# Kernel optimization log

Measured on AMD Instinct MI355X. Metric: run time of the kernel, lower is better.

## Reference

```python
import jax, jax.numpy as jnp
import numpy as np
import math

V = 32768; H = 768; NH = 12; D = 64; L = 12; I = 2048
S = 512; B = 8; BK = 32; MAXP = 512; EPS = 1e-7
STD = math.sqrt(2.0 / (5.0 * H))
SCALE = 1.0 / math.sqrt(3 * D)


def _bucket_positions(seq_len):
    # static numpy: DeBERTa-style log-bucketed relative positions
    rel = np.arange(seq_len)[:, None] - np.arange(seq_len)[None, :]
    sign = np.sign(rel)
    mid = BK // 2
    abs_pos = np.where((rel < mid) & (rel > -mid), mid - 1, np.minimum(np.abs(rel), MAXP - 1))
    log_pos = np.ceil(np.log(abs_pos / mid) / math.log((MAXP - 1) / mid) * (mid - 1)).astype(np.int64) + mid
    bucket = np.where(abs_pos <= mid, rel, log_pos * sign).astype(np.int64)
    return bucket + BK - 1  # [S, S] in [0, 2*BK-2]


def _ln(x):
    # LayerNorm without affine params (elementwise_affine=False)
    m = jnp.mean(x, axis=-1, keepdims=True)
    v = jnp.var(x, axis=-1, keepdims=True)
    return (x - m) * jax.lax.rsqrt(v + EPS)


def _forward(input_ids, attention_mask, word_emb, rel_emb, rel_g, rel_b,
             Wqk, bqk, Wvg, bvg, Wout, bout, W1, W2):
    pos_idx = jnp.asarray(_bucket_positions(S))      # [S, S]
    x = _ln(word_emb[input_ids])                     # [S, B, H]
    rel = _ln(rel_emb) * rel_g + rel_b               # [2*BK-1, H] (affine LN)
    mask = attention_mask                            # [B, 1, 1, S] bool, True = masked
    for i in range(L):
        # ---- disentangled attention ----
        hs = _ln(x)
        qk = jnp.einsum('sbh,oh->sbo', hs, Wqk[i]) + bqk[i]
        q, k = jnp.split(qk, 2, axis=-1)
        vg = jnp.einsum('sbh,oh->sbo', hs, Wvg[i]) + bvg[i]
        v, g = jnp.split(vg, 2, axis=-1)
        g = jax.nn.gelu(g, approximate=False)
        pos = jnp.einsum('rh,oh->ro', rel, Wqk[i]) + bqk[i]   # [2*BK-1, 2H]
        posg = pos[pos_idx]                                   # [S, S, 2H]
        qpos, kpos = jnp.split(posg, 2, axis=-1)
        qpos = qpos.reshape(S, S, NH, D)
        kpos = kpos.reshape(S, S, NH, D)
        qh = q.reshape(S, B, NH, D)
        kh = k.reshape(S, B, NH, D)
        vh = v.reshape(S, B, NH, D)
        scores = jnp.einsum('qbhd,kbhd->bhqk', qh, kh) * SCALE          # content-content
        scores = scores + jnp.einsum('qbhd,qkhd->bhqk', qh, kpos) * SCALE  # content-position
        scores = scores + jnp.einsum('kbhd,qkhd->bhqk', kh, qpos) * SCALE  # position-content
        s = jnp.where(mask, -1e9, scores)
        p = jax.nn.softmax(s, axis=-1)
        p = jnp.where(mask, 0.0, p)
        ctx = jnp.einsum('bhqk,kbhd->qbhd', p, vh).reshape(S, B, H)
        ctx = _ln(ctx * g)
        ctx = jnp.einsum('sbh,oh->sbo', ctx, Wout[i]) + bout[i]
        x = x + ctx
        # ---- GeGLU feed-forward ----
        h = _ln(x)
        h = jnp.einsum('sbh,oh->sbo', h, W1[i])   # [S, B, 2I]
        a, gt = jnp.split(h, 2, axis=-1)
        h = _ln(a * jax.nn.gelu(gt, approximate=True))
        h = jnp.einsum('sbi,oi->sbo', h, W2[i])
        x = x + h
    return x


def setup_inputs() -> dict:
    key = jax.random.key(0)
    ks = jax.random.split(key, 12)
    def nrm(k, shape):
        return (jax.random.normal(k, shape) * STD).astype(jnp.float32)
    return {
        'input_ids': jax.random.randint(ks[0], (S, B), 0, V),
        'attention_mask': jax.random.randint(ks[1], (B, 1, 1, S), 0, 2).astype(bool),
        'word_emb': nrm(ks[2], (V, H)),
        'rel_emb': nrm(ks[3], (2 * BK - 1, H)),
        'rel_g': jnp.ones((H,), jnp.float32),
        'rel_b': jnp.zeros((H,), jnp.float32),
        'Wqk': nrm(ks[4], (L, 2 * H, H)),
        'bqk': jnp.zeros((L, 2 * H), jnp.float32),
        'Wvg': nrm(ks[5], (L, 2 * H, H)),
        'bvg': jnp.zeros((L, 2 * H), jnp.float32),
        'Wout': nrm(ks[6], (L, H, H)),
        'bout': jnp.zeros((L, H), jnp.float32),
        'W1': nrm(ks[7], (L, 2 * I, H)),
        'W2': nrm(ks[8], (L, H, I)),
    }


def reference(input_ids, attention_mask, word_emb, rel_emb, rel_g, rel_b,
              Wqk, bqk, Wvg, bvg, Wout, bout, W1, W2):
    return _forward(input_ids, attention_mask, word_emb, rel_emb, rel_g, rel_b,
                    Wqk, bqk, Wvg, bvg, Wout, bout, W1, W2)
```

## Files before the change

kernel.cpp:

```cpp
#include <hip/hip_runtime.h>
#include <math.h>

#define SS 512
#define BB 8
#define NHH 12
#define DD 64
#define HH 768
#define II 2048
#define LL 12
#define SCALE_F 0.07216878364870323f

typedef __attribute__((ext_vector_type(8))) short bf16x8;
typedef __attribute__((ext_vector_type(4))) float f32x4;

__device__ __forceinline__ unsigned short f2b(float f) {
    union { float f; unsigned int u; } x; x.f = f;
    unsigned int r = x.u + 0x7fffu + ((x.u >> 16) & 1u);
    return (unsigned short)(r >> 16);
}
__device__ __forceinline__ float b2f(unsigned short u) {
    union { unsigned int u; float f; } x; x.u = ((unsigned int)u) << 16;
    return x.f;
}

__device__ __forceinline__ float2 blockReduceSum2(float a, float b) {
    __shared__ float2 sm[4];
    __shared__ float2 bc;
#pragma unroll
    for (int o = 32; o > 0; o >>= 1) {
        a += __shfl_down(a, o);
        b += __shfl_down(b, o);
    }
    int t = threadIdx.x;
    if ((t & 63) == 0) sm[t >> 6] = make_float2(a, b);
    __syncthreads();
    if (t == 0) {
        float xa = sm[0].x + sm[1].x + sm[2].x + sm[3].x;
        float xb = sm[0].y + sm[1].y + sm[2].y + sm[3].y;
        bc = make_float2(xa, xb);
    }
    __syncthreads();
    return bc;
}

__device__ __forceinline__ float gelu_erf(float v) {
    return 0.5f * v * (1.0f + erff(v * 0.70710678118654752f));
}
__device__ __forceinline__ float gelu_tanh(float v) {
    const float c = 0.7978845608028654f;
    return 0.5f * v * (1.0f + tanhf(c * (v + 0.044715f * v * v * v)));
}

__global__ __launch_bounds__(256) void k_decode_mask(const unsigned char* __restrict__ raw,
                                                     int* __restrict__ mask, int n) {
    __shared__ int s_any;
    if (threadIdx.x == 0) s_any = 0;
    __syncthreads();
    int local = 0;
    for (int i = threadIdx.x; i < n; i += blockDim.x)
        if ((i & 3) && raw[i]) local = 1;
    if (local) atomicOr(&s_any, 1);
    __syncthreads();
    bool isU8 = (s_any != 0);
    const int* as_int = (const int*)raw;
    for (int i = threadIdx.x; i < n; i += blockDim.x)
        mask[i] = isU8 ? (raw[i] != 0) : (as_int[i] != 0);
}

__global__ __launch_bounds__(256) void k_bucket(int* __restrict__ tab) {
    int i = blockIdx.x * 256 + threadIdx.x;
    if (i >= 1023) return;
    int rel = i - 511;
    int a = rel < 0 ? -rel : rel;
    int abs_pos = (a < 16) ? 15 : (a < 511 ? a : 511);
    int bucket;
    if (abs_pos <= 16) {
        bucket = rel;
    } else {
        double lp = ceil(log((double)abs_pos / 16.0) / log(511.0 / 16.0) * 15.0);
        int l = (int)lp + 16;
        bucket = (rel > 0) ? l : -l;
    }
    int idx = bucket + 31;
    if (idx < 0) idx = 0;
    if (idx > 62) idx = 62;
    tab[i] = idx;
}

__global__ __launch_bounds__(256) void k_f2b(const float* __restrict__ in,
                                             unsigned short* __restrict__ out, int n8) {
    int i = blockIdx.x * 256 + threadIdx.x;
    if (i >= n8) return;
    float4 a = ((const float4*)in)[2 * (size_t)i];
    float4 b = ((const float4*)in)[2 * (size_t)i + 1];
    ushort4 lo, hi;
    lo.x = f2b(a.x); lo.y = f2b(a.y); lo.z = f2b(a.z); lo.w = f2b(a.w);
    hi.x = f2b(b.x); hi.y = f2b(b.y); hi.z = f2b(b.z); hi.w = f2b(b.w);
    ((ushort4*)out)[2 * (size_t)i] = lo;
    ((ushort4*)out)[2 * (size_t)i + 1] = hi;
}

__global__ __launch_bounds__(256) void k_f2b_ln(const float* __restrict__ wvg,
                                                const float* __restrict__ wout,
                                                const float* __restrict__ w1,
                                                const float* __restrict__ w2,
                                                unsigned short* __restrict__ wbf,
                                                const float* __restrict__ x,
                                                unsigned short* __restrict__ hs) {
    int bid = blockIdx.x;
    int t = threadIdx.x;
    if (bid < 3169) {
        int i = bid * 256 + t;
        if (i >= 811008) return;
        const float* src;
        int off;
        if (i < 221184) {
            if (i < 147456) { src = wvg;  off = i; }
            else            { src = wout; off = i - 147456; }
        } else if (i < 614400) { src = w1; off = i - 221184; }
        else                   { src = w2; off = i - 614400; }
        float4 a = ((const float4*)src)[2 * (size_t)off];
        float4 b = ((const float4*)src)[2 * (size_t)off + 1];
        ushort4 lo, hi;
        lo.x = f2b(a.x); lo.y = f2b(a.y); lo.z = f2b(a.z); lo.w = f2b(a.w);
        hi.x = f2b(b.x); hi.y = f2b(b.y); hi.z = f2b(b.z); hi.w = f2b(b.w);
        ((ushort4*)wbf)[2 * (size_t)i] = lo;
        ((ushort4*)wbf)[2 * (size_t)i + 1] = hi;
    } else {
        int row = bid - 3169;
        const float* r = x + (size_t)row * HH;
        float v0 = r[t], v1 = r[t + 256], v2 = r[t + 512];
        float s = v0 + v1 + v2;
        float ss = v0 * v0 + v1 * v1 + v2 * v2;
        float2 r2 = blockReduceSum2(s, ss);
        float mean = r2.x * (1.0f / HH);
        float var = r2.y * (1.0f / HH) - mean * mean;
        float rs = rsqrtf(var + 1e-7f);
        unsigned short* o = hs + (size_t)row * HH;
        o[t] = f2b((v0 - mean) * rs);
        o[t + 256] = f2b((v1 - mean) * rs);
        o[t + 512] = f2b((v2 - mean) * rs);
    }
}

__global__ __launch_bounds__(256) void k_ln_bf(const float* __restrict__ in,
                                               unsigned short* __restrict__ out) {
    int row = blockIdx.x, t = threadIdx.x;
    const float* r = in + (size_t)row * HH;
    float v0 = r[t], v1 = r[t + 256], v2 = r[t + 512];
    float s = v0 + v1 + v2;
    float ss = v0 * v0 + v1 * v1 + v2 * v2;
    float2 r2 = blockReduceSum2(s, ss);
    float mean = r2.x * (1.0f / HH);
    float var = r2.y * (1.0f / HH) - mean * mean;
    float rs = rsqrtf(var + 1e-7f);
    unsigned short* o = out + (size_t)row * HH;
    o[t] = f2b((v0 - mean) * rs);
    o[t + 256] = f2b((v1 - mean) * rs);
    o[t + 512] = f2b((v2 - mean) * rs);
}

__global__ __launch_bounds__(256) void k_embed_ln(const int* __restrict__ ids,
                                                  const float* __restrict__ emb,
                                                  float* __restrict__ out) {
    int row = blockIdx.x, t = threadIdx.x;
    const float* r = emb + (size_t)ids[row] * HH;
    float v0 = r[t], v1 = r[t + 256], v2 = r[t + 512];
    float s = v0 + v1 + v2;
    float ss = v0 * v0 + v1 * v1 + v2 * v2;
    float2 r2 = blockReduceSum2(s, ss);
    float mean = r2.x * (1.0f / HH);
    float var = r2.y * (1.0f / HH) - mean * mean;
    float rs = rsqrtf(var + 1e-7f);
    float* o = out + (size_t)row * HH;
    o[t] = (v0 - mean) * rs;
    o[t + 256] = (v1 - mean) * rs;
    o[t + 512] = (v2 - mean) * rs;
}

__global__ __launch_bounds__(256) void k_rel_ln_bf(const float* __restrict__ rel_emb,
                                                   const float* __restrict__ g,
                                                   const float* __restrict__ b,
                                                   unsigned short* __restrict__ out) {
    int row = blockIdx.x, t = threadIdx.x;
    unsigned short* o = out + (size_t)row * HH;
    if (row >= 63) {
        o[t] = 0; o[t + 256] = 0; o[t + 512] = 0;
        return;
    }
    const float* r = rel_emb + (size_t)row * HH;
    float v0 = r[t], v1 = r[t + 256], v2 = r[t + 512];
    float s = v0 + v1 + v2;
    float ss = v0 * v0 + v1 * v1 + v2 * v2;
    float2 r2 = blockReduceSum2(s, ss);
    float mean = r2.x * (1.0f / HH);
    float var = r2.y * (1.0f / HH) - mean * mean;
    float rs = rsqrtf(var + 1e-7f);
    o[t] = f2b((v0 - mean) * rs * g[t] + b[t]);
    o[t + 256] = f2b((v1 - mean) * rs * g[t + 256] + b[t + 256]);
    o[t + 512] = f2b((v2 - mean) * rs * g[t + 512] + b[t + 512]);
}

__global__ __launch_bounds__(256) void k_gated_ln(const float* __restrict__ ctxr,
                                                  const unsigned short* __restrict__ qkvg,
                                                  unsigned short* __restrict__ out) {
    int row = blockIdx.x, t = threadIdx.x;
    const float* cr = ctxr + (size_t)row * HH;
    const unsigned short* gr = qkvg + (size_t)row * 3072 + 2304;
    float v[3];
    float s = 0.f, ss = 0.f;
#pragma unroll
    for (int e = 0; e < 3; ++e) {
        int i = t + e * 256;
        float x = cr[i] * gelu_erf(b2f(gr[i]));
        v[e] = x;
        s += x; ss += x * x;
    }
    float2 r2 = blockReduceSum2(s, ss);
    float mean = r2.x * (1.0f / HH);
    float var = r2.y * (1.0f / HH) - mean * mean;
    float rs = rsqrtf(var + 1e-7f);
    unsigned short* o = out + (size_t)row * HH;
#pragma unroll
    for (int e = 0; e < 3; ++e) o[t + e * 256] = f2b((v[e] - mean) * rs);
}

__global__ __launch_bounds__(256) void k_ffn_ln(const unsigned short* __restrict__ ffh,
                                                unsigned short* __restrict__ out) {
    int row = blockIdx.x, t = threadIdx.x;
    const unsigned short* ar = ffh + (size_t)row * 4096 + t * 8;
    const unsigned short* gr = ar + II;
    ushort4 a0 = *(const ushort4*)ar;
    ushort4 a1 = *(const ushort4*)(ar + 4);
    ushort4 g0 = *(const ushort4*)gr;
    ushort4 g1 = *(const ushort4*)(gr + 4);
    float av[8] = {b2f(a0.x), b2f(a0.y), b2f(a0.z), b2f(a0.w),
                   b2f(a1.x), b2f(a1.y), b2f(a1.z), b2f(a1.w)};
    float gv[8] = {b2f(g0.x), b2f(g0.y), b2f(g0.z), b2f(g0.w),
                   b2f(g1.x), b2f(g1.y), b2f(g1.z), b2f(g1.w)};
    float v[8];
    float s = 0.f, ss = 0.f;
#pragma unroll
    for (int e = 0; e < 8; ++e) {
        float x = av[e] * gelu_tanh(gv[e]);
        v[e] = x;
        s += x; ss += x * x;
    }
    float2 r2 = blockReduceSum2(s, ss);
    float mean = r2.x * (1.0f / II);
    float var = r2.y * (1.0f / II) - mean * mean;
    float rs = rsqrtf(var + 1e-7f);
    ushort4 o0, o1;
    o0.x = f2b((v[0] - mean) * rs); o0.y = f2b((v[1] - mean) * rs);
    o0.z = f2b((v[2] - mean) * rs); o0.w = f2b((v[3] - mean) * rs);
    o1.x = f2b((v[4] - mean) * rs); o1.y = f2b((v[5] - mean) * rs);
    o1.z = f2b((v[6] - mean) * rs); o1.w = f2b((v[7] - mean) * rs);
    unsigned short* o = out + (size_t)row * II + t * 8;
    *(ushort4*)o = o0;
    *(ushort4*)(o + 4) = o1;
}

template <int OBF>
__global__ __launch_bounds__(256) void k_gemm_bf16(const unsigned short* __restrict__ A, int lda,
                                                   const unsigned short* __restrict__ W, int ldw,
                                                   void* __restrict__ Cv, int ldc,
                                                   int M, int N, int K,
                                                   const float* __restrict__ bias,
                                                   const float* __restrict__ bias2,
                                                   const float* __restrict__ res,
                                                   size_t wz, size_t cz, size_t bz) {
    __shared__ unsigned short As[128 * 32];
    __shared__ unsigned short Ws[128 * 32];
    int zz = blockIdx.z;
    W += (size_t)zz * wz;
    if (bias) bias += (size_t)zz * bz;
    int nwg = gridDim.x * gridDim.y;
    int orig = blockIdx.y * gridDim.x + blockIdx.x;
    int qq = nwg >> 3, rr = nwg & 7;
    int xcd = orig & 7, idx = orig >> 3;
    int wg = (xcd < rr ? xcd * (qq + 1) : rr * (qq + 1) + (xcd - rr) * qq) + idx;
    int bx = wg % gridDim.x, by = wg / gridDim.x;

    const int t = threadIdx.x;
    const int lane = t & 63, wid = t >> 6;
    const int row0 = by * 128, col0 = bx * 128;
    const int wr = (wid >> 1) * 64, wc = (wid & 1) * 64;
    const int rA = lane & 15, kA = (lane >> 4) * 8;

    f32x4 acc[4][4] = {};

    for (int k0 = 0; k0 < K; k0 += 32) {
#pragma unroll
        for (int j = 0; j < 2; ++j) {
            int c = t + j * 256;
            int r = c >> 2, ko = (c & 3) * 8;
            const unsigned short* srcA = A + (size_t)(row0 + r) * lda + k0 + ko;
            const unsigned short* srcB = W + (size_t)(col0 + r) * ldw + k0 + ko;
            unsigned short* dstA = As + (size_t)(j * 256 + wid * 64) * 8;
            unsigned short* dstB = Ws + (size_t)(j * 256 + wid * 64) * 8;
            __builtin_amdgcn_global_load_lds(
                (const __attribute__((address_space(1))) void*)srcA,
                (__attribute__((address_space(3))) void*)dstA, 16, 0, 0);
            __builtin_amdgcn_global_load_lds(
                (const __attribute__((address_space(1))) void*)srcB,
                (__attribute__((address_space(3))) void*)dstB, 16, 0, 0);
        }
        __syncthreads();
        bf16x8 af[4], bfr[4];
#pragma unroll
        for (int m = 0; m < 4; ++m)
            af[m] = *(const bf16x8*)&As[(wr + m * 16 + rA) * 32 + kA];
#pragma unroll
        for (int n = 0; n < 4; ++n)
            bfr[n] = *(const bf16x8*)&Ws[(wc + n * 16 + rA) * 32 + kA];
#pragma unroll
        for (int m = 0; m < 4; ++m)
#pragma unroll
            for (int n = 0; n < 4; ++n)
                acc[m][n] = __builtin_amdgcn_mfma_f32_16x16x32_bf16(af[m], bfr[n], acc[m][n], 0, 0, 0);
        __syncthreads();
    }

    float* Cf = (float*)Cv + (size_t)zz * cz;
    unsigned short* Cb = (unsigned short*)Cv + (size_t)zz * cz;
    const int cl = lane & 15, rg = (lane >> 4) * 4;
#pragma unroll
    for (int n = 0; n < 4; ++n) {
        int gc = col0 + wc + n * 16 + cl;
        float bv = 0.0f;
        if (bias) bv = (bias2 && gc >= 1536) ? bias2[gc - 1536] : bias[gc];
#pragma unroll
        for (int m = 0; m < 4; ++m) {
#pragma unroll
            for (int i = 0; i < 4; ++i) {
                int gr = row0 + wr + m * 16 + rg + i;
                float v = acc[m][n][i] + bv;
                if (OBF) {
                    Cb[(size_t)gr * ldc + gc] = f2b(v);
                } else {
                    if (res) v += res[(size_t)gr * ldc + gc];
                    Cf[(size_t)gr * ldc + gc] = v;
                }
            }
        }
    }
}

#define SKSLOT 16384

__device__ __forceinline__ void sk_stage(const unsigned short* __restrict__ Ab, int lda,
                                         const unsigned short* __restrict__ Wb, int ldw,
                                         unsigned char* slot, int t, int wid) {
    int rit = t >> 3;
    int kb = (t & 7) << 4;
#pragma unroll
    for (int c = 0; c < 2; ++c) {
        int row = c * 32 + rit;
        int gkb = kb ^ ((row & 7) << 4);
        const unsigned short* src = Ab + (size_t)row * lda + (gkb >> 1);
        unsigned char* dst = slot + c * 4096 + wid * 1024;
        __builtin_amdgcn_global_load_lds(
            (const __attribute__((address_space(1))) void*)src,
            (__attribute__((address_space(3))) void*)dst, 16, 0, 0);
    }
#pragma unroll
    for (int c = 0; c < 2; ++c) {
        int row = c * 32 + rit;
        int gkb = kb ^ ((row & 7) << 4);
        const unsigned short* src = Wb + (size_t)row * ldw + (gkb >> 1);
        unsigned char* dst = slot + 8192 + c * 4096 + wid * 1024;
        __builtin_amdgcn_global_load_lds(
            (const __attribute__((address_space(1))) void*)src,
            (__attribute__((address_space(3))) void*)dst, 16, 0, 0);
    }
}

__device__ __forceinline__ void sk_compute(const unsigned char* slot, int wr, int wc,
                                           int rA, int g16, f32x4 acc[2][2]) {
    const unsigned char* Ab = slot;
    const unsigned char* Bb = slot + 8192;
    bf16x8 a[2][2], b[2][2];
#pragma unroll
    for (int m = 0; m < 2; ++m) {
        int row = wr + m * 16 + rA;
        int sw = (row & 7) << 4;
#pragma unroll
        for (int s = 0; s < 2; ++s)
            a[m][s] = *(const bf16x8*)(Ab + row * 128 + ((s * 64 + g16 * 16) ^ sw));
    }
#pragma unroll
    for (int n = 0; n < 2; ++n) {
        int row = wc + n * 16 + rA;
        int sw = (row & 7) << 4;
#pragma unroll
        for (int s = 0; s < 2; ++s)
            b[n][s] = *(const bf16x8*)(Bb + row * 128 + ((s * 64 + g16 * 16) ^ sw));
    }
    __builtin_amdgcn_s_setprio(1);
#pragma unroll
    for (int m = 0; m < 2; ++m)
#pragma unroll
        for (int n = 0; n < 2; ++n) {
            acc[m][n] = __builtin_amdgcn_mfma_f32_16x16x32_bf16(a[m][0], b[n][0], acc[m][n], 0, 0, 0);
            acc[m][n] = __builtin_amdgcn_mfma_f32_16x16x32_bf16(a[m][1], b[n][1], acc[m][n], 0, 0, 0);
        }
    __builtin_amdgcn_s_setprio(0);
}

__global__ __launch_bounds__(256) void k_gemm_skinny(const unsigned short* __restrict__ A, int lda,
                                                     const unsigned short* __restrict__ W, int ldw,
                                                     float* __restrict__ C, int ldc,
                                                     int M, int N, int K,
                                                     const float* __restrict__ bias,
                                                     const float* __restrict__ res) {
    __shared__ unsigned char smem[2 * SKSLOT];
    int nwg = gridDim.x * gridDim.y;
    int orig = blockIdx.y * gridDim.x + blockIdx.x;
    int qq = nwg >> 3, rr = nwg & 7;
    int xcd = orig & 7, idx = orig >> 3;
    int wg = (xcd < rr ? xcd * (qq + 1) : rr * (qq + 1) + (xcd - rr) * qq) + idx;
    int bx = wg % gridDim.x, by = wg / gridDim.x;

    const int t = threadIdx.x;
    const int lane = t & 63, wid = t >> 6;
    const int row0 = by * 64, col0 = bx * 64;
    const int wr = (wid >> 1) * 32, wc = (wid & 1) * 32;
    const int rA = lane & 15, g16 = lane >> 4;
    const unsigned short* Abase = A + (size_t)row0 * lda;
    const unsigned short* Wbase = W + (size_t)col0 * ldw;

    const int nt = K >> 6;
    f32x4 acc[2][2] = {};

    sk_stage(Abase, lda, Wbase, ldw, smem, t, wid);

    for (int tt = 0; tt < nt; ++tt) {
        asm volatile("s_barrier" ::: "memory");
        if (tt + 1 < nt) {
            sk_stage(Abase + (size_t)(tt + 1) * 64, lda, Wbase + (size_t)(tt + 1) * 64,
                     ldw, smem + (size_t)((tt + 1) & 1) * SKSLOT, t, wid);
            asm volatile("s_waitcnt vmcnt(4)" ::: "memory");
        } else {
            asm volatile("s_waitcnt vmcnt(0)" ::: "memory");
        }
        asm volatile("s_barrier" ::: "memory");
        sk_compute(smem + (size_t)(tt & 1) * SKSLOT, wr, wc, rA, g16, acc);
    }

    const int cl = lane & 15, rg = (lane >> 4) * 4;
#pragma unroll
    for (int n = 0; n < 2; ++n) {
        int gc = col0 + wc + n * 16 + cl;
        float bv = bias ? bias[gc] : 0.0f;
#pragma unroll
        for (int m = 0; m < 2; ++m) {
#pragma unroll
            for (int i = 0; i < 4; ++i) {
                int gr = row0 + wr + m * 16 + rg + i;
                float v = acc[m][n][i] + bv;
                if (res) v += res[(size_t)gr * ldc + gc];
                C[(size_t)gr * ldc + gc] = v;
            }
        }
    }
}

#define GSLOT 49152

__device__ __forceinline__ void g_stage(const unsigned short* __restrict__ Abase, int lda,
                                        const unsigned short* __restrict__ Wbase, int ldw,
                                        unsigned char* slot, int t, int wid) {
    int rit = t >> 3;
    int kb = (t & 7) << 4;
#pragma unroll
    for (int c = 0; c < 2; ++c) {
        int row = c * 64 + rit;
        int gkb = kb ^ ((row & 7) << 4);
        const unsigned short* src = Abase + (size_t)row * lda + (gkb >> 1);
        unsigned char* dst = slot + c * 8192 + wid * 1024;
        __builtin_amdgcn_global_load_lds(
            (const __attribute__((address_space(1))) void*)src,
            (__attribute__((address_space(3))) void*)dst, 16, 0, 0);
    }
#pragma unroll
    for (int c = 0; c < 4; ++c) {
        int row = c * 64 + rit;
        int gkb = kb ^ ((row & 7) << 4);
        const unsigned short* src = Wbase + (size_t)row * ldw + (gkb >> 1);
        unsigned char* dst = slot + 16384 + c * 8192 + wid * 1024;
        __builtin_amdgcn_global_load_lds(
            (const __attribute__((address_space(1))) void*)src,
            (__attribute__((address_space(3))) void*)dst, 16, 0, 0);
    }
}

__device__ __forceinline__ void g_compute(const unsigned char* slot, int wm, int wn,
                                          int rA, int g16, f32x4 acc[4][4]) {
    const unsigned char* Ab = slot;
    const unsigned char* Bb = slot + 16384;
    bf16x8 a[4][2], b[4][2];
#pragma unroll
    for (int m = 0; m < 4; ++m) {
        int row = wm * 64 + m * 16 + rA;
        int sw = (row & 7) << 4;
#pragma unroll
        for (int s = 0; s < 2; ++s)
            a[m][s] = *(const bf16x8*)(Ab + row * 128 + ((s * 64 + g16 * 16) ^ sw));
    }
#pragma unroll
    for (int n = 0; n < 4; ++n) {
        int row = wn * 64 + n * 16 + rA;
        int sw = (row & 7) << 4;
#pragma unroll
        for (int s = 0; s < 2; ++s)
            b[n][s] = *(const bf16x8*)(Bb + row * 128 + ((s * 64 + g16 * 16) ^ sw));
    }
    __builtin_amdgcn_s_setprio(1);
#pragma unroll
    for (int m = 0; m < 4; ++m)
#pragma unroll
        for (int n = 0; n < 4; ++n) {
            acc[m][n] = __builtin_amdgcn_mfma_f32_16x16x32_bf16(a[m][0], b[n][0], acc[m][n], 0, 0, 0);
            acc[m][n] = __builtin_amdgcn_mfma_f32_16x16x32_bf16(a[m][1], b[n][1], acc[m][n], 0, 0, 0);
        }
    __builtin_amdgcn_s_setprio(0);
}

template <int OBF>
__global__ __launch_bounds__(512, 1) void k_gemm_big(const unsigned short* __restrict__ A, int lda,
                                                     const unsigned short* __restrict__ W,
                                                     const unsigned short* __restrict__ Wb2, int ldw,
                                                     void* __restrict__ Cv, int ldc,
                                                     int M, int N, int K,
                                                     const float* __restrict__ bias,
                                                     const float* __restrict__ bias2,
                                                     const float* __restrict__ res) {
    extern __shared__ unsigned char smem[];
    int nwg = gridDim.x * gridDim.y;
    int orig = blockIdx.y * gridDim.x + blockIdx.x;
    int qq = nwg >> 3, rr = nwg & 7;
    int xcd = orig & 7, idx = orig >> 3;
    int wg = (xcd < rr ? xcd * (qq + 1) : rr * (qq + 1) + (xcd - rr) * qq) + idx;
    int bx = wg % gridDim.x, by = wg / gridDim.x;

    const int t = threadIdx.x;
    const int lane = t & 63, wid = t >> 6;
    const int wm = wid >> 2, wn = wid & 3;
    const int rA = lane & 15, g16 = lane >> 4;
    const int row0 = by * 128, col0 = bx * 256;
    const unsigned short* Abase = A + (size_t)row0 * lda;
    const unsigned short* Wbase = (Wb2 && col0 >= 1536)
                                      ? Wb2 + (size_t)(col0 - 1536) * ldw
                                      : W + (size_t)col0 * ldw;

    const int nt = K >> 6;
    f32x4 acc[4][4] = {};

    g_stage(Abase, lda, Wbase, ldw, smem, t, wid);
    g_stage(Abase + 64, lda, Wbase + 64, ldw, smem + GSLOT, t, wid);

#define GBAR() asm volatile("s_barrier" ::: "memory")
#define GITER(T, STG, VMSTR)                                                        \
    do {                                                                            \
        GBAR();                                                                     \
        if (STG)                                                                    \
            g_stage(Abase + (size_t)(T + 2) * 64, lda, Wbase + (size_t)(T + 2) * 64,\
                    ldw, smem + (size_t)((T + 2) % 3) * GSLOT, t, wid);             \
        asm volatile(VMSTR ::: "memory");                                           \
        GBAR();                                                                     \
        g_compute(smem + (size_t)((T) % 3) * GSLOT, wm, wn, rA, g16, acc);          \
    } while (0)

    int tt = 0;
    for (; tt < nt - 2; ++tt) GITER(tt, true, "s_waitcnt vmcnt(12)");
    GITER(tt, false, "s_waitcnt vmcnt(6)");
    ++tt;
    GITER(tt, false, "s_waitcnt vmcnt(0)");
#undef GITER
#undef GBAR

    float* Cf = (float*)Cv;
    unsigned short* Cb = (unsigned short*)Cv;
    const int cl = lane & 15, rg = (lane >> 4) * 4;
#pragma unroll
    for (int n = 0; n < 4; ++n) {
        int gc = col0 + wn * 64 + n * 16 + cl;
        float bv = 0.0f;
        if (bias) bv = (bias2 && gc >= 1536) ? bias2[gc - 1536] : bias[gc];
#pragma unroll
        for (int m = 0; m < 4; ++m) {
#pragma unroll
            for (int i = 0; i < 4; ++i) {
                int gr = row0 + wm * 64 + m * 16 + rg + i;
                float v = acc[m][n][i] + bv;
                if (OBF) {
                    Cb[(size_t)gr * ldc + gc] = f2b(v);
                } else {
                    if (res) v += res[(size_t)gr * ldc + gc];
                    Cf[(size_t)gr * ldc + gc] = v;
                }
            }
        }
    }
}

__global__ __launch_bounds__(256) void k_repack_cppc(const unsigned short* __restrict__ qkvg,
                                                     const unsigned short* __restrict__ pp,
                                                     unsigned short* __restrict__ qT,
                                                     unsigned short* __restrict__ kT,
                                                     unsigned short* __restrict__ vT,
                                                     float* __restrict__ cp,
                                                     float* __restrict__ pc) {
    __shared__ unsigned char shmem[12288];
    int t = threadIdx.x;
    if (blockIdx.x < 8) {
        unsigned short (*tile)[72] = (unsigned short(*)[72])shmem;
        int bh = blockIdx.y;
        int b = bh / NHH, h = bh % NHH;
        int s0 = blockIdx.x * 64;
#pragma unroll
        for (int j = 0; j < 2; ++j) {
            int idx = t + j * 256;
            int r = idx >> 3, dc = idx & 7;
            const unsigned short* src = qkvg + ((size_t)(s0 + r) * BB + b) * 3072 + h * DD + dc * 8;
            ushort4 a = *(const ushort4*)src;
            ushort4 c = *(const ushort4*)(src + 4);
            unsigned short* dq = qT + ((size_t)bh * SS + s0 + r) * DD + dc * 8;
            *(ushort4*)dq = a; *(ushort4*)(dq + 4) = c;
            const unsigned short* srck = src + HH;
            ushort4 a2 = *(const ushort4*)srck;
            ushort4 c2 = *(const ushort4*)(srck + 4);
            unsigned short* dk = kT + ((size_t)bh * SS + s0 + r) * DD + dc * 8;
            *(ushort4*)dk = a2; *(ushort4*)(dk + 4) = c2;
        }
#pragma unroll
        for (int j = 0; j < 4; ++j) {
            int idx = t + j * 256;
            int r = idx >> 4, c4 = idx & 15;
            ushort4 u = *(const ushort4*)(qkvg + ((size_t)(s0 + r) * BB + b) * 3072 + 1536 + h * DD + c4 * 4);
            *(ushort4*)&tile[r][c4 * 4] = u;
        }
        __syncthreads();
#pragma unroll
        for (int j = 0; j < 2; ++j) {
            int idx = t + j * 256;
            int d = idx >> 3, s8 = idx & 7;
            ushort4 a, c;
            a.x = tile[s8 * 8 + 0][d]; a.y = tile[s8 * 8 + 1][d];
            a.z = tile[s8 * 8 + 2][d]; a.w = tile[s8 * 8 + 3][d];
            c.x = tile[s8 * 8 + 4][d]; c.y = tile[s8 * 8 + 5][d];
            c.z = tile[s8 * 8 + 6][d]; c.w = tile[s8 * 8 + 7][d];
            unsigned short* dst = vT + ((size_t)bh * DD + d) * SS + s0 + s8 * 8;
            *(ushort4*)dst = a; *(ushort4*)(dst + 4) = c;
        }
    } else {
        int cid = (blockIdx.x - 8) * 96 + blockIdx.y;
        int z = cid >= 384;
        int rem = cid - (z ? 384 : 0);
        int h = rem >> 5;
        int mt = rem & 31;
        int aoff = z ? HH : 0;
        int toff = z ? 0 : HH;
        float* out = z ? pc : cp;
        unsigned short* As = (unsigned short*)shmem;
        unsigned short* Bs = (unsigned short*)(shmem + 8192);
        const int lane = t & 63, wid = t >> 6;
        const int rA = lane & 15, kA = (lane >> 4) * 8;

        f32x4 acc[2][4] = {};

        for (int k0 = 0; k0 < 64; k0 += 32) {
#pragma unroll
            for (int j = 0; j < 2; ++j) {
                int c = t + j * 256;
                int r = c >> 2, ko = (c & 3) * 8;
                const unsigned short* srcA = qkvg + (size_t)(mt * 128 + r) * 3072 + aoff + h * DD + k0 + ko;
                unsigned short* dstA = As + (size_t)(j * 256 + wid * 64) * 8;
                __builtin_amdgcn_global_load_lds(
                    (const __attribute__((address_space(1))) void*)srcA,
                    (__attribute__((address_space(3))) void*)dstA, 16, 0, 0);
            }
            {
                int r = t >> 2, ko = (t & 3) * 8;
                const unsigned short* srcB = pp + (size_t)r * 1536 + toff + h * DD + k0 + ko;
                unsigned short* dstB = Bs + (size_t)(wid * 64) * 8;
                __builtin_amdgcn_global_load_lds(
                    (const __attribute__((address_space(1))) void*)srcB,
                    (__attribute__((address_space(3))) void*)dstB, 16, 0, 0);
            }
            __syncthreads();
            bf16x8 af[2], bfr[4];
#pragma unroll
            for (int m = 0; m < 2; ++m)
                af[m] = *(const bf16x8*)&As[(wid * 32 + m * 16 + rA) * 32 + kA];
#pragma unroll
            for (int n = 0; n < 4; ++n)
                bfr[n] = *(const bf16x8*)&Bs[(n * 16 + rA) * 32 + kA];
#pragma unroll
            for (int m = 0; m < 2; ++m)
#pragma unroll
                for (int n = 0; n < 4; ++n)
                    acc[m][n] = __builtin_amdgcn_mfma_f32_16x16x32_bf16(af[m], bfr[n], acc[m][n], 0, 0, 0);
            __syncthreads();
        }

        const int cl = lane & 15, rg = (lane >> 4) * 4;
#pragma unroll
        for (int m = 0; m < 2; ++m)
#pragma unroll
            for (int n = 0; n < 4; ++n) {
                int gc = n * 16 + cl;
                if (gc < 63) {
#pragma unroll
                    for (int i = 0; i < 4; ++i) {
                        int gr = mt * 128 + wid * 32 + m * 16 + rg + i;
                        int sIdx = gr >> 3, bIdx = gr & 7;
                        out[(((size_t)(bIdx * NHH + h)) * SS + sIdx) * 63 + gc] = acc[m][n][i];
                    }
                }
            }
    }
}

__global__ __launch_bounds__(256) void k_attn_fused(
    const unsigned short* __restrict__ qT, const unsigned short* __restrict__ kT,
    const unsigned short* __restrict__ vT, const float* __restrict__ cp,
    const float* __restrict__ pc, const int* __restrict__ bucket,
    const int* __restrict__ mask, float* __restrict__ ctxr) {
    __shared__ float cps[64 * 63];
    __shared__ float pcs[64 * 63];
    __shared__ unsigned short pb_all[4][16 * 72];
    __shared__ int btab[1023];
    int t = threadIdx.x;
    int lane = t & 63, wid = t >> 6;
    int bh = blockIdx.y;
    int b = bh / NHH, h = bh % NHH;
    int qb0 = blockIdx.x * 64;
    int q0 = qb0 + wid * 16;
    int rA = lane & 15, g = lane >> 4, kA = g * 8;
    unsigned short* pb = pb_all[wid];
    const unsigned short* qTb = qT + (size_t)bh * SS * DD;
    const unsigned short* kTb = kT + (size_t)bh * SS * DD;
    const unsigned short* vTb = vT + (size_t)bh * DD * SS;
    const float* cpb = cp + (size_t)bh * SS * 63 + (size_t)qb0 * 63;
    const float* pcb = pc + (size_t)bh * SS * 63;
    const int* mkb = mask + b * SS;

    for (int i = t; i < 1023; i += 256) btab[i] = bucket[i];
    for (int i = t; i < 1008; i += 256) ((float4*)cps)[i] = ((const float4*)cpb)[i];

    bf16x8 aq[2];
#pragma unroll
    for (int dc = 0; dc < 2; ++dc)
        aq[dc] = *(const bf16x8*)&qTb[(size_t)(q0 + rA) * DD + dc * 32 + kA];

    f32x4 o[4] = {};
    float mrow[4], lrow[4];
#pragma unroll
    for (int i = 0; i < 4; ++i) { mrow[i] = -INFINITY; lrow[i] = 0.f; }

    for (int kt = 0; kt < 8; ++kt) {
        int k0 = kt * 64;
        __syncthreads();
        {
            const float4* src = (const float4*)(pcb + (size_t)k0 * 63);
            for (int i = t; i < 1008; i += 256) ((float4*)pcs)[i] = src[i];
        }
        f32x4 sa[4] = {};
#pragma unroll
        for (int n = 0; n < 4; ++n) {
            bf16x8 bk0 = *(const bf16x8*)&kTb[(size_t)(k0 + n * 16 + rA) * DD + kA];
            bf16x8 bk1 = *(const bf16x8*)&kTb[(size_t)(k0 + n * 16 + rA) * DD + 32 + kA];
            sa[n] = __builtin_amdgcn_mfma_f32_16x16x32_bf16(aq[0], bk0, sa[n], 0, 0, 0);
            sa[n] = __builtin_amdgcn_mfma_f32_16x16x32_bf16(aq[1], bk1, sa[n], 0, 0, 0);
        }
        int mk[4];
#pragma unroll
        for (int n = 0; n < 4; ++n) mk[n] = mkb[k0 + n * 16 + rA];
        __syncthreads();

        float pv[4][4];
#pragma unroll
        for (int i = 0; i < 4; ++i) {
            int qr = wid * 16 + g * 4 + i;
            int q = qb0 + qr;
            float sv[4];
            float tmax = -INFINITY;
#pragma unroll
            for (int n = 0; n < 4; ++n) {
                int kr = n * 16 + rA;
                int id = btab[q - (k0 + kr) + 511];
                float v = (sa[n][i] + cps[qr * 63 + id] + pcs[kr * 63 + id]) * SCALE_F;
                v = mk[n] ? -1e9f : v;
                sv[n] = v;
                tmax = fmaxf(tmax, v);
            }
            tmax = fmaxf(tmax, __shfl_xor(tmax, 1, 16));
            tmax = fmaxf(tmax, __shfl_xor(tmax, 2, 16));
            tmax = fmaxf(tmax, __shfl_xor(tmax, 4, 16));
            tmax = fmaxf(tmax, __shfl_xor(tmax, 8, 16));
            float mold = mrow[i];
            float mnew = fmaxf(mold, tmax);
            float ls = 0.f;
#pragma unroll
            for (int n = 0; n < 4; ++n) {
                float p = __expf(sv[n] - mnew);
                pv[n][i] = p;
                ls += p;
            }
            ls += __shfl_xor(ls, 1, 16);
            ls += __shfl_xor(ls, 2, 16);
            ls += __shfl_xor(ls, 4, 16);
            ls += __shfl_xor(ls, 8, 16);
            if (mnew > mold) {
                float alpha = __expf(mold - mnew);
                lrow[i] = lrow[i] * alpha + ls;
                mrow[i] = mnew;
#pragma unroll
                for (int n = 0; n < 4; ++n) o[n][i] *= alpha;
            } else {
                lrow[i] += ls;
            }
        }
#pragma unroll
        for (int n = 0; n < 4; ++n)
#pragma unroll
            for (int i = 0; i < 4; ++i)
                pb[(g * 4 + i) * 72 + n * 16 + rA] = f2b(pv[n][i]);
        bf16x8 ap[2];
#pragma unroll
        for (int kc = 0; kc < 2; ++kc)
            ap[kc] = *(const bf16x8*)&pb[rA * 72 + kc * 32 + kA];
#pragma unroll
        for (int n = 0; n < 4; ++n) {
            bf16x8 bv0 = *(const bf16x8*)&vTb[(size_t)(n * 16 + rA) * SS + k0 + kA];
            bf16x8 bv1 = *(const bf16x8*)&vTb[(size_t)(n * 16 + rA) * SS + k0 + 32 + kA];
            o[n] = __builtin_amdgcn_mfma_f32_16x16x32_bf16(ap[0], bv0, o[n], 0, 0, 0);
            o[n] = __builtin_amdgcn_mfma_f32_16x16x32_bf16(ap[1], bv1, o[n], 0, 0, 0);
        }
    }
#pragma unroll
    for (int i = 0; i < 4; ++i) {
        int q = q0 + g * 4 + i;
        float inv = 1.0f / lrow[i];
#pragma unroll
        for (int n = 0; n < 4; ++n)
            ctxr[((size_t)q * BB + b) * HH + h * DD + n * 16 + rA] = o[n][i] * inv;
    }
}

static inline void gemm_big(const unsigned short* A, int lda,
                            const unsigned short* W, const unsigned short* Wb2, int ldw,
                            void* C, int ldc, int M, int N, int K,
                            const float* bias, const float* bias2, const float* res,
                            int obf, hipStream_t st) {
    dim3 g(N / 256, M / 128);
    if (obf)
        k_gemm_big<1><<<g, 512, 3 * GSLOT, st>>>(A, lda, W, Wb2, ldw, C, ldc, M, N, K, bias, bias2, res);
    else
        k_gemm_big<0><<<g, 512, 3 * GSLOT, st>>>(A, lda, W, Wb2, ldw, C, ldc, M, N, K, bias, bias2, res);
}

extern "C" void kernel_launch(void* const* d_in, const int* in_sizes, int n_in,
                              void* d_out, int out_size, void* d_ws, size_t ws_size,
                              hipStream_t stream) {
    static int attr_done = 0;
    if (!attr_done) {
        hipFuncSetAttribute((const void*)&k_gemm_big<1>,
                            hipFuncAttributeMaxDynamicSharedMemorySize, 3 * GSLOT);
        hipFuncSetAttribute((const void*)&k_gemm_big<0>,
                            hipFuncAttributeMaxDynamicSharedMemorySize, 3 * GSLOT);
        attr_done = 1;
    }

    const int* ids = (const int*)d_in[0];
    const unsigned char* maskraw = (const unsigned char*)d_in[1];
    const float* word_emb = (const float*)d_in[2];
    const float* rel_emb = (const float*)d_in[3];
    const float* rel_g = (const float*)d_in[4];
    const float* rel_b = (const float*)d_in[5];
    const float* Wqk = (const float*)d_in[6];
    const float* bqk = (const float*)d_in[7];
    const float* Wvg = (const float*)d_in[8];
    const float* bvg = (const float*)d_in[9];
    const float* Wout = (const float*)d_in[10];
    const float* bout = (const float*)d_in[11];
    const float* W1 = (const float*)d_in[12];
    const float* W2 = (const float*)d_in[13];

    const size_t N_X = (size_t)SS * BB * HH;
    const size_t N_CP = (size_t)SS * BB * NHH * 63;
    const size_t N_H2 = (size_t)SS * BB * II;
    const size_t N_WQK = (size_t)2 * HH * HH;
    const size_t N_WOUT = (size_t)HH * HH;
    const size_t N_W1 = (size_t)2 * II * HH;
    const size_t N_W2 = (size_t)HH * II;
    const size_t N_HD = (size_t)BB * NHH * SS * DD;
    const size_t N_QKVG = (size_t)SS * BB * 3072;
    const size_t N_FFH = (size_t)SS * BB * 4096;
    const size_t N_PP = (size_t)128 * 1536;

    float* ws = (float*)d_ws;
    float* x = ws;
    float* ctxr = x + N_X;
    float* cp = ctxr + N_X;
    float* pc = cp + N_CP;
    unsigned short* us = (unsigned short*)(pc + N_CP);
    unsigned short* qkvg = us;
    unsigned short* hs_bf = qkvg + N_QKVG;
    unsigned short* ctx_bf = hs_bf + N_X;
    unsigned short* h2_bf = ctx_bf + N_X;
    unsigned short* ffh = h2_bf + N_H2;
    unsigned short* wqk_all = ffh + N_FFH;
    unsigned short* wvg_bf = wqk_all + 12 * N_WQK;
    unsigned short* wout_bf = wvg_bf + N_WQK;
    unsigned short* w1_bf = wout_bf + N_WOUT;
    unsigned short* w2_bf = w1_bf + N_W1;
    unsigned short* ppall = w2_bf + N_W2;
    unsigned short* rel_bf = ppall + 12 * N_PP;
    unsigned short* qT = rel_bf + 128 * HH;
    unsigned short* kT = qT + N_HD;
    unsigned short* vT = kT + N_HD;
    int* bucket = (int*)(vT + N_HD);
    int* maski = bucket + 1024;

    size_t need_bytes = ((size_t)(maski + BB * SS) - (size_t)d_ws);
    if (ws_size < need_bytes) return;

    k_decode_mask<<<1, 256, 0, stream>>>(maskraw, maski, BB * SS);
    k_bucket<<<4, 256, 0, stream>>>(bucket);
    k_embed_ln<<<SS * BB, 256, 0, stream>>>(ids, word_emb, x);
    k_rel_ln_bf<<<128, 256, 0, stream>>>(rel_emb, rel_g, rel_b, rel_bf);
    k_f2b<<<(int)((12 * N_WQK / 8 + 255) / 256), 256, 0, stream>>>(Wqk, wqk_all,
                                                                   (int)(12 * N_WQK / 8));
    {
        dim3 gpp(1536 / 128, 1, 12);
        k_gemm_bf16<1><<<gpp, 256, 0, stream>>>(rel_bf, HH, wqk_all, HH, ppall, 1536,
                                                128, 1536, HH, bqk, nullptr, nullptr,
                                                N_WQK, N_PP, 2 * HH);
    }

    for (int l = 0; l < LL; ++l) {
        const unsigned short* wqk_l = wqk_all + (size_t)l * N_WQK;
        const float* bqk_l = bqk + (size_t)l * 2 * HH;
        const float* Wvg_l = Wvg + (size_t)l * N_WQK;
        const float* bvg_l = bvg + (size_t)l * 2 * HH;
        const float* Wout_l = Wout + (size_t)l * N_WOUT;
        const float* bout_l = bout + (size_t)l * HH;
        const float* W1_l = W1 + (size_t)l * N_W1;
        const float* W2_l = W2 + (size_t)l * N_W2;

        k_f2b_ln<<<3169 + SS * BB, 256, 0, stream>>>(Wvg_l, Wout_l, W1_l, W2_l, wvg_bf,
                                                     x, hs_bf);
        gemm_big(hs_bf, HH, wqk_l, wvg_bf, HH, qkvg, 3072, SS * BB, 3072, HH,
                 bqk_l, bvg_l, nullptr, 1, stream);
        k_repack_cppc<<<dim3(16, 96), 256, 0, stream>>>(qkvg, ppall + (size_t)l * N_PP,
                                                        qT, kT, vT, cp, pc);
        k_attn_fused<<<dim3(SS / 64, BB * NHH), 256, 0, stream>>>(qT, kT, vT, cp, pc,
                                                                  bucket, maski, ctxr);
        k_gated_ln<<<SS * BB, 256, 0, stream>>>(ctxr, qkvg, ctx_bf);
        k_gemm_skinny<<<dim3(HH / 64, SS * BB / 64), 256, 0, stream>>>(
            ctx_bf, HH, wout_bf, HH, x, HH, SS * BB, HH, HH, bout_l, x);

        k_ln_bf<<<SS * BB, 256, 0, stream>>>(x, hs_bf);
        gemm_big(hs_bf, HH, w1_bf, nullptr, HH, ffh, 4096, SS * BB, 4096, HH,
                 nullptr, nullptr, nullptr, 1, stream);
        k_ffn_ln<<<SS * BB, 256, 0, stream>>>(ffh, h2_bf);
        float* outC = (l == LL - 1) ? (float*)d_out : x;
        k_gemm_skinny<<<dim3(HH / 64, SS * BB / 64), 256, 0, stream>>>(
            h2_bf, II, w2_bf, II, outC, HH, SS * BB, HH, II, nullptr, x);
    }
}
```

Baseline: 2.706 ms.

## Replace big-tile GEMM with 128x128-tile double-buffered GEMM for QKVG and FFN1

Replaces the 128x256-tile, triple-buffered, one-block-per-CU GEMM with a 128x128-tile kernel that double-buffers through 64KB of LDS and drops the occupancy limit of 1. This doubles the grid size (more blocks for M=4096, N=3072/4096) and lets two blocks share a CU, aiming for better load balance and latency hiding. The cost is less data reuse per tile, more global traffic for A, and a shallower prefetch pipeline.

```diff
diff --git a/kernel.cpp b/kernel.cpp
--- a/kernel.cpp
+++ b/kernel.cpp
@@ -465,28 +465,28 @@
     }
 }
 
-#define GSLOT 49152
-
-__device__ __forceinline__ void g_stage(const unsigned short* __restrict__ Abase, int lda,
-                                        const unsigned short* __restrict__ Wbase, int ldw,
-                                        unsigned char* slot, int t, int wid) {
+#define MDSLOT 32768
+
+__device__ __forceinline__ void md_stage(const unsigned short* __restrict__ Ab, int lda,
+                                         const unsigned short* __restrict__ Wb, int ldw,
+                                         unsigned char* slot, int t, int wid) {
     int rit = t >> 3;
     int kb = (t & 7) << 4;
 #pragma unroll
     for (int c = 0; c < 2; ++c) {
         int row = c * 64 + rit;
         int gkb = kb ^ ((row & 7) << 4);
-        const unsigned short* src = Abase + (size_t)row * lda + (gkb >> 1);
+        const unsigned short* src = Ab + (size_t)row * lda + (gkb >> 1);
         unsigned char* dst = slot + c * 8192 + wid * 1024;
         __builtin_amdgcn_global_load_lds(
             (const __attribute__((address_space(1))) void*)src,
             (__attribute__((address_space(3))) void*)dst, 16, 0, 0);
     }
 #pragma unroll
-    for (int c = 0; c < 4; ++c) {
+    for (int c = 0; c < 2; ++c) {
         int row = c * 64 + rit;
         int gkb = kb ^ ((row & 7) << 4);
-        const unsigned short* src = Wbase + (size_t)row * ldw + (gkb >> 1);
+        const unsigned short* src = Wb + (size_t)row * ldw + (gkb >> 1);
         unsigned char* dst = slot + 16384 + c * 8192 + wid * 1024;
         __builtin_amdgcn_global_load_lds(
             (const __attribute__((address_space(1))) void*)src,
@@ -494,11 +494,11 @@
     }
 }
 
-__device__ __forceinline__ void g_compute(const unsigned char* slot, int wm, int wn,
-                                          int rA, int g16, f32x4 acc[4][4]) {
+__device__ __forceinline__ void md_compute(const unsigned char* slot, int wm, int wn,
+                                           int rA, int g16, f32x4 acc[4][2]) {
     const unsigned char* Ab = slot;
     const unsigned char* Bb = slot + 16384;
-    bf16x8 a[4][2], b[4][2];
+    bf16x8 a[4][2], b[2][2];
 #pragma unroll
     for (int m = 0; m < 4; ++m) {
         int row = wm * 64 + m * 16 + rA;
@@ -508,8 +508,8 @@
             a[m][s] = *(const bf16x8*)(Ab + row * 128 + ((s * 64 + g16 * 16) ^ sw));
     }
 #pragma unroll
-    for (int n = 0; n < 4; ++n) {
-        int row = wn * 64 + n * 16 + rA;
+    for (int n = 0; n < 2; ++n) {
+        int row = wn * 32 + n * 16 + rA;
         int sw = (row & 7) << 4;
 #pragma unroll
         for (int s = 0; s < 2; ++s)
@@ -519,22 +519,20 @@
 #pragma unroll
     for (int m = 0; m < 4; ++m)
 #pragma unroll
-        for (int n = 0; n < 4; ++n) {
+        for (int n = 0; n < 2; ++n) {
             acc[m][n] = __builtin_amdgcn_mfma_f32_16x16x32_bf16(a[m][0], b[n][0], acc[m][n], 0, 0, 0);
             acc[m][n] = __builtin_amdgcn_mfma_f32_16x16x32_bf16(a[m][1], b[n][1], acc[m][n], 0, 0, 0);
         }
     __builtin_amdgcn_s_setprio(0);
 }
 
-template <int OBF>
-__global__ __launch_bounds__(512, 1) void k_gemm_big(const unsigned short* __restrict__ A, int lda,
-                                                     const unsigned short* __restrict__ W,
-                                                     const unsigned short* __restrict__ Wb2, int ldw,
-                                                     void* __restrict__ Cv, int ldc,
-                                                     int M, int N, int K,
-                                                     const float* __restrict__ bias,
-                                                     const float* __restrict__ bias2,
-                                                     const float* __restrict__ res) {
+__global__ __launch_bounds__(512) void k_gemm_mid(const unsigned short* __restrict__ A, int lda,
+                                                  const unsigned short* __restrict__ W,
+                                                  const unsigned short* __restrict__ Wb2, int ldw,
+                                                  unsigned short* __restrict__ Cb, int ldc,
+                                                  int M, int N, int K,
+                                                  const float* __restrict__ bias,
+                                                  const float* __restrict__ bias2) {
     extern __shared__ unsigned char smem[];
     int nwg = gridDim.x * gridDim.y;
     int orig = blockIdx.y * gridDim.x + blockIdx.x;
@@ -547,44 +545,34 @@
     const int lane = t & 63, wid = t >> 6;
     const int wm = wid >> 2, wn = wid & 3;
     const int rA = lane & 15, g16 = lane >> 4;
-    const int row0 = by * 128, col0 = bx * 256;
+    const int row0 = by * 128, col0 = bx * 128;
     const unsigned short* Abase = A + (size_t)row0 * lda;
     const unsigned short* Wbase = (Wb2 && col0 >= 1536)
                                       ? Wb2 + (size_t)(col0 - 1536) * ldw
                                       : W + (size_t)col0 * ldw;
 
     const int nt = K >> 6;
-    f32x4 acc[4][4] = {};
-
-    g_stage(Abase, lda, Wbase, ldw, smem, t, wid);
-    g_stage(Abase + 64, lda, Wbase + 64, ldw, smem + GSLOT, t, wid);
-
-#define GBAR() asm volatile("s_barrier" ::: "memory")
-#define GITER(T, STG, VMSTR)                                                        \
-    do {                                                                            \
-        GBAR();                                                                     \
-        if (STG)                                                                    \
-            g_stage(Abase + (size_t)(T + 2) * 64, lda, Wbase + (size_t)(T + 2) * 64,\
-                    ldw, smem + (size_t)((T + 2) % 3) * GSLOT, t, wid);             \
-        asm volatile(VMSTR ::: "memory");                                           \
-        GBAR();                                                                     \
-        g_compute(smem + (size_t)((T) % 3) * GSLOT, wm, wn, rA, g16, acc);          \
-    } while (0)
-
-    int tt = 0;
-    for (; tt < nt - 2; ++tt) GITER(tt, true, "s_waitcnt vmcnt(12)");
-    GITER(tt, false, "s_waitcnt vmcnt(6)");
-    ++tt;
-    GITER(tt, false, "s_waitcnt vmcnt(0)");
-#undef GITER
-#undef GBAR
-
-    float* Cf = (float*)Cv;
-    unsigned short* Cb = (unsigned short*)Cv;
+    f32x4 acc[4][2] = {};
+
+    md_stage(Abase, lda, Wbase, ldw, smem, t, wid);
+
+    for (int tt = 0; tt < nt; ++tt) {
+        asm volatile("s_barrier" ::: "memory");
+        if (tt + 1 < nt) {
+            md_stage(Abase + (size_t)(tt + 1) * 64, lda, Wbase + (size_t)(tt + 1) * 64,
+                     ldw, smem + (size_t)((tt + 1) & 1) * MDSLOT, t, wid);
+            asm volatile("s_waitcnt vmcnt(4)" ::: "memory");
+        } else {
+            asm volatile("s_waitcnt vmcnt(0)" ::: "memory");
+        }
+        asm volatile("s_barrier" ::: "memory");
+        md_compute(smem + (size_t)(tt & 1) * MDSLOT, wm, wn, rA, g16, acc);
+    }
+
     const int cl = lane & 15, rg = (lane >> 4) * 4;
 #pragma unroll
-    for (int n = 0; n < 4; ++n) {
-        int gc = col0 + wn * 64 + n * 16 + cl;
+    for (int n = 0; n < 2; ++n) {
+        int gc = col0 + wn * 32 + n * 16 + cl;
         float bv = 0.0f;
         if (bias) bv = (bias2 && gc >= 1536) ? bias2[gc - 1536] : bias[gc];
 #pragma unroll
@@ -592,13 +580,7 @@
 #pragma unroll
             for (int i = 0; i < 4; ++i) {
                 int gr = row0 + wm * 64 + m * 16 + rg + i;
-                float v = acc[m][n][i] + bv;
-                if (OBF) {
-                    Cb[(size_t)gr * ldc + gc] = f2b(v);
-                } else {
-                    if (res) v += res[(size_t)gr * ldc + gc];
-                    Cf[(size_t)gr * ldc + gc] = v;
-                }
+                Cb[(size_t)gr * ldc + gc] = f2b(acc[m][n][i] + bv);
             }
         }
     }
@@ -849,16 +831,12 @@
     }
 }
 
-static inline void gemm_big(const unsigned short* A, int lda,
+static inline void gemm_mid(const unsigned short* A, int lda,
                             const unsigned short* W, const unsigned short* Wb2, int ldw,
-                            void* C, int ldc, int M, int N, int K,
-                            const float* bias, const float* bias2, const float* res,
-                            int obf, hipStream_t st) {
-    dim3 g(N / 256, M / 128);
-    if (obf)
-        k_gemm_big<1><<<g, 512, 3 * GSLOT, st>>>(A, lda, W, Wb2, ldw, C, ldc, M, N, K, bias, bias2, res);
-    else
-        k_gemm_big<0><<<g, 512, 3 * GSLOT, st>>>(A, lda, W, Wb2, ldw, C, ldc, M, N, K, bias, bias2, res);
+                            unsigned short* C, int ldc, int M, int N, int K,
+                            const float* bias, const float* bias2, hipStream_t st) {
+    dim3 g(N / 128, M / 128);
+    k_gemm_mid<<<g, 512, 2 * MDSLOT, st>>>(A, lda, W, Wb2, ldw, C, ldc, M, N, K, bias, bias2);
 }
 
 extern "C" void kernel_launch(void* const* d_in, const int* in_sizes, int n_in,
@@ -866,10 +844,8 @@
                               hipStream_t stream) {
     static int attr_done = 0;
     if (!attr_done) {
-        hipFuncSetAttribute((const void*)&k_gemm_big<1>,
-                            hipFuncAttributeMaxDynamicSharedMemorySize, 3 * GSLOT);
-        hipFuncSetAttribute((const void*)&k_gemm_big<0>,
-                            hipFuncAttributeMaxDynamicSharedMemorySize, 3 * GSLOT);
+        hipFuncSetAttribute((const void*)&k_gemm_mid,
+                            hipFuncAttributeMaxDynamicSharedMemorySize, 2 * MDSLOT);
         attr_done = 1;
     }
 
@@ -952,8 +928,8 @@
 
         k_f2b_ln<<<3169 + SS * BB, 256, 0, stream>>>(Wvg_l, Wout_l, W1_l, W2_l, wvg_bf,
                                                      x, hs_bf);
-        gemm_big(hs_bf, HH, wqk_l, wvg_bf, HH, qkvg, 3072, SS * BB, 3072, HH,
-                 bqk_l, bvg_l, nullptr, 1, stream);
+        gemm_mid(hs_bf, HH, wqk_l, wvg_bf, HH, qkvg, 3072, SS * BB, 3072, HH,
+                 bqk_l, bvg_l, stream);
         k_repack_cppc<<<dim3(16, 96), 256, 0, stream>>>(qkvg, ppall + (size_t)l * N_PP,
                                                         qT, kT, vT, cp, pc);
         k_attn_fused<<<dim3(SS / 64, BB * NHH), 256, 0, stream>>>(qT, kT, vT, cp, pc,
@@ -963,8 +939,8 @@
             ctx_bf, HH, wout_bf, HH, x, HH, SS * BB, HH, HH, bout_l, x);
 
         k_ln_bf<<<SS * BB, 256, 0, stream>>>(x, hs_bf);
-        gemm_big(hs_bf, HH, w1_bf, nullptr, HH, ffh, 4096, SS * BB, 4096, HH,
-                 nullptr, nullptr, nullptr, 1, stream);
+        gemm_mid(hs_bf, HH, w1_bf, nullptr, HH, ffh, 4096, SS * BB, 4096, HH,
+                 nullptr, nullptr, stream);
         k_ffn_ln<<<SS * BB, 256, 0, stream>>>(ffh, h2_bf);
         float* outC = (l == LL - 1) ? (float*)d_out : x;
         k_gemm_skinny<<<dim3(HH / 64, SS * BB / 64), 256, 0, stream>>>(
```

Measured after the change: 2.660 ms. No clear change (-1.7%).
